# Kernel optimization log

Measured on AMD Instinct MI355X. Metric: run time of the kernel, lower is better.

Reference implementation:

```python
import jax, jax.numpy as jnp
import numpy as np

SCENE = (256, 256, 32)     # scene_size from SLCF-Net docstring (256*256*32 voxels)
PROJECT_SCALE = 1
C, H, W = 64, 480, 640
N = SCENE[0] * SCENE[1] * SCENE[2]


def setup_inputs() -> dict:
    key = jax.random.key(0)
    k1, k2, k3, k4, k5 = jax.random.split(key, 5)
    x2d = jax.random.normal(k1, (C, H, W), dtype=jnp.float32)
    # pix coords in [0, 480) -> valid for both x (<640) and y (<480)
    projected_pix = jax.random.randint(k2, (N, 2), 0, 480, dtype=jnp.int32)
    fov_mask = jax.random.bernoulli(k3, 0.7, (N,))
    pix_z = jax.random.uniform(k4, (N,), dtype=jnp.float32) * 50.0
    depth_img = jax.random.uniform(k5, (1, H, W), dtype=jnp.float32) * 50.0
    return {
        "x2d": x2d,
        "projected_pix": projected_pix,
        "scale_2d": 1,
        "fov_mask": fov_mask,
        "pix_z": pix_z,
        "depth_img": depth_img,
    }


def reference(x2d, projected_pix, scale_2d, fov_mask, pix_z, depth_img):
    c, h, w = x2d.shape
    pix_x = projected_pix[:, 0]
    pix_y = projected_pix[:, 1]

    # --- feature gather (out-of-FOV voxels map to the appended zero column) ---
    sx = pix_x // scale_2d
    sy = pix_y // scale_2d
    feat_idx = sy * w + sx                                  # (N,)
    src = x2d.reshape(c, -1)                                # (c, h*w)
    src_feature = jnp.where(fov_mask[None, :], src[:, feat_idx], jnp.float32(0.0))  # (c, N)

    # --- depth gather (out-of-FOV voxels map to the appended zero entry) ---
    dep_idx = pix_y * w + pix_x                             # (N,)
    depth_flat = depth_img.reshape(-1)                      # (h*w,)
    depth_values = jnp.where(fov_mask, depth_flat[dep_idx], jnp.float32(0.0))       # (N,)

    # --- gaussian decay weight, mu=0, sigma=1/project_scale; depth==0 -> weight 1 ---
    sigma = jnp.float32(1.0 / PROJECT_SCALE)
    gw = jnp.exp(jnp.float32(-0.5) * ((pix_z - depth_values) / sigma) ** 2)
    weights = jnp.where(depth_values == 0.0, jnp.float32(1.0), gw)                  # (N,)

    weighted = src_feature * weights[None, :]               # (c, N)
    s = PROJECT_SCALE
    return weighted.reshape(c, SCENE[0] // s, SCENE[1] // s, SCENE[2] // s)
```

## Files before the change

kernel.cpp:

```cpp
#include <hip/hip_runtime.h>
#include <hip/hip_bf16.h>

#define NVOX (256*256*32)
#define CC 64
#define HH 480
#define WW 640
#define HWTOT (HH*WW)

typedef float vfloat4 __attribute__((ext_vector_type(4)));
typedef int   vint4   __attribute__((ext_vector_type(4)));

__global__ __launch_bounds__(256) void weight_kernel(
    const int*   __restrict__ pp,
    const int*   __restrict__ scale_p,
    const int*   __restrict__ mask,
    const float* __restrict__ pix_z,
    const float* __restrict__ depth,
    int*         __restrict__ feat_out,
    float*       __restrict__ w_out)
{
    int t = blockIdx.x * blockDim.x + threadIdx.x;
    if (t * 4 >= NVOX) return;
    int scale = scale_p[0];

    vint4 pp0 = ((const vint4*)pp)[t*2+0];
    vint4 pp1 = ((const vint4*)pp)[t*2+1];
    vint4 m4  = ((const vint4*)mask)[t];
    vfloat4 z4 = ((const vfloat4*)pix_z)[t];

    int   px[4] = {pp0.x, pp0.z, pp1.x, pp1.z};
    int   py[4] = {pp0.y, pp0.w, pp1.y, pp1.w};
    int   mm[4] = {m4.x, m4.y, m4.z, m4.w};
    float zz[4] = {z4.x, z4.y, z4.z, z4.w};

    int fi[4]; float wv[4];
#pragma unroll
    for (int j = 0; j < 4; ++j) {
        int sx = px[j], sy = py[j];
        if (scale != 1) { sx = px[j] / scale; sy = py[j] / scale; }
        int feat = sy * WW + sx;
        bool fov = (mm[j] != 0);
        float d = fov ? depth[py[j] * WW + px[j]] : 0.0f;
        float diff = zz[j] - d;
        float gw = __expf(-0.5f * diff * diff);
        float w = (d == 0.0f) ? 1.0f : gw;
        wv[j] = fov ? w : 0.0f;
        fi[j] = fov ? feat : 0;
    }
    vint4 fo;  fo.x=fi[0]; fo.y=fi[1]; fo.z=fi[2]; fo.w=fi[3];
    vfloat4 wo; wo.x=wv[0]; wo.y=wv[1]; wo.z=wv[2]; wo.w=wv[3];
    ((vint4*)feat_out)[t] = fo;
    ((vfloat4*)w_out)[t]  = wo;
}

__global__ __launch_bounds__(256) void transpose_kernel(
    const float* __restrict__ x2d,
    float*       __restrict__ xT)
{
    __shared__ float tile[64][65];
    int t  = threadIdx.x;
    int p0 = blockIdx.x * 64;

#pragma unroll
    for (int k = 0; k < 16; ++k) {
        int c = k * 4 + (t >> 6);
        int p = t & 63;
        tile[c][p] = x2d[(long)c * HWTOT + p0 + p];
    }
    __syncthreads();
#pragma unroll
    for (int k = 0; k < 16; ++k) {
        int p = k * 4 + (t >> 6);
        int c = t & 63;
        xT[(long)(p0 + p) * CC + c] = tile[c][p];
    }
}

__global__ __launch_bounds__(256) void gather64_kernel(
    const float* __restrict__ xT,
    const int*   __restrict__ feat_idx,
    const float* __restrict__ wgt,
    float*       __restrict__ out)
{
    int i = blockIdx.x * blockDim.x + threadIdx.x;
    int fi  = __builtin_nontemporal_load(feat_idx + i);
    float w = __builtin_nontemporal_load(wgt + i);

    const vfloat4* src = (const vfloat4*)(xT + (long)fi * CC);
    float* op = out + i;

#pragma unroll
    for (int g = 0; g < 16; ++g) {
        vfloat4 v = src[g];
        v.x *= w; v.y *= w; v.z *= w; v.w *= w;
        __builtin_nontemporal_store(v.x, op + (long)(4*g + 0) * NVOX);
        __builtin_nontemporal_store(v.y, op + (long)(4*g + 1) * NVOX);
        __builtin_nontemporal_store(v.z, op + (long)(4*g + 2) * NVOX);
        __builtin_nontemporal_store(v.w, op + (long)(4*g + 3) * NVOX);
    }
}

__global__ __launch_bounds__(256) void scatter_kernel(
    const float* __restrict__ x2d,
    const int*   __restrict__ feat_idx,
    const float* __restrict__ wgt,
    float*       __restrict__ out)
{
    int t = blockIdx.x * blockDim.x + threadIdx.x;
    long i0 = (long)t * 4;
    int cg = blockIdx.y * 4;

    vint4   f4 = __builtin_nontemporal_load((const vint4*)feat_idx + t);
    vfloat4 w4 = __builtin_nontemporal_load((const vfloat4*)wgt + t);

#pragma unroll
    for (int g = 0; g < 4; ++g) {
        int c = cg + g;
        const float* base = x2d + (long)c * HWTOT;
        vfloat4 v;
        v.x = base[f4.x] * w4.x;
        v.y = base[f4.y] * w4.y;
        v.z = base[f4.z] * w4.z;
        v.w = base[f4.w] * w4.w;
        __builtin_nontemporal_store(v, (vfloat4*)(out + (long)c * NVOX + i0));
    }
}

__global__ __launch_bounds__(256) void fused_kernel(
    const float* __restrict__ x2d,
    const int*   __restrict__ pp,
    const int*   __restrict__ scale_p,
    const int*   __restrict__ mask,
    const float* __restrict__ pix_z,
    const float* __restrict__ depth,
    float*       __restrict__ out)
{
    int t = blockIdx.x * blockDim.x + threadIdx.x;
    long i0 = (long)t * 4;
    int cg = blockIdx.y * 4;
    int scale = scale_p[0];

    vint4 pp0 = ((const vint4*)pp)[t*2+0];
    vint4 pp1 = ((const vint4*)pp)[t*2+1];
    vint4 m4  = ((const vint4*)mask)[t];
    vfloat4 z4 = ((const vfloat4*)pix_z)[t];

    int   px[4] = {pp0.x, pp0.z, pp1.x, pp1.z};
    int   py[4] = {pp0.y, pp0.w, pp1.y, pp1.w};
    int   mm[4] = {m4.x, m4.y, m4.z, m4.w};
    float zz[4] = {z4.x, z4.y, z4.z, z4.w};

    int fi[4]; float wv[4];
#pragma unroll
    for (int j = 0; j < 4; ++j) {
        int sx = px[j], sy = py[j];
        if (scale != 1) { sx = px[j] / scale; sy = py[j] / scale; }
        int feat = sy * WW + sx;
        bool fov = (mm[j] != 0);
        float d = fov ? depth[py[j] * WW + px[j]] : 0.0f;
        float diff = zz[j] - d;
        float gw = __expf(-0.5f * diff * diff);
        float w = (d == 0.0f) ? 1.0f : gw;
        wv[j] = fov ? w : 0.0f;
        fi[j] = fov ? feat : 0;
    }

#pragma unroll
    for (int g = 0; g < 4; ++g) {
        int c = cg + g;
        const float* base = x2d + (long)c * HWTOT;
        vfloat4 v;
        v.x = base[fi[0]] * wv[0];
        v.y = base[fi[1]] * wv[1];
        v.z = base[fi[2]] * wv[2];
        v.w = base[fi[3]] * wv[3];
        __builtin_nontemporal_store(v, (vfloat4*)(out + (long)c * NVOX + i0));
    }
}

extern "C" void kernel_launch(void* const* d_in, const int* in_sizes, int n_in,
                              void* d_out, int out_size, void* d_ws, size_t ws_size,
                              hipStream_t stream) {
    const float* x2d     = (const float*)d_in[0];
    const int*   pp      = (const int*)d_in[1];
    const int*   scale_p = (const int*)d_in[2];
    const int*   mask    = (const int*)d_in[3];
    const float* pix_z   = (const float*)d_in[4];
    const float* depth   = (const float*)d_in[5];
    float*       out     = (float*)d_out;

    const int nquad = NVOX / 4;
    dim3 blk(256);

    size_t need_meta = (size_t)NVOX * 8;
    size_t need_full = need_meta + (size_t)HWTOT * CC * 4;

    if (ws_size >= need_full) {
        int*   feat_ws = (int*)d_ws;
        float* w_ws    = (float*)((char*)d_ws + (size_t)NVOX * 4);
        float* xT      = (float*)((char*)d_ws + need_meta);
        weight_kernel<<<dim3(nquad/256), blk, 0, stream>>>(pp, scale_p, mask,
                                                           pix_z, depth, feat_ws, w_ws);
        transpose_kernel<<<dim3(HWTOT/64), blk, 0, stream>>>(x2d, xT);
        gather64_kernel<<<dim3(NVOX/256), blk, 0, stream>>>(xT, feat_ws, w_ws, out);
    } else if (ws_size >= need_meta) {
        int*   feat_ws = (int*)d_ws;
        float* w_ws    = (float*)((char*)d_ws + (size_t)NVOX * 4);
        weight_kernel<<<dim3(nquad/256), blk, 0, stream>>>(pp, scale_p, mask,
                                                           pix_z, depth, feat_ws, w_ws);
        scatter_kernel<<<dim3(nquad/256, CC/4), blk, 0, stream>>>(x2d, feat_ws, w_ws, out);
    } else {
        fused_kernel<<<dim3(nquad/256, CC/4), blk, 0, stream>>>(x2d, pp, scale_p,
                                                                mask, pix_z, depth, out);
    }
}
```

Measured before the change: 663.0 us.

## Fuse weight computation into gather kernel and vectorize transpose loads/stores

Drops the separate weight/index kernel and computes each voxel's feature index and Gaussian depth weight inside the gather kernel. This avoids writing and re-reading two N-sized metadata arrays and saves one launch. The transpose kernel now uses float4 nontemporal loads and float4 stores, so each thread moves four values per access. Shared-memory reads in the transpose now stride across channels, which may cause some bank conflicts.

Result: slower. 688.6 us (+3.9%).

```diff
diff --git a/kernel.cpp b/kernel.cpp
--- a/kernel.cpp
+++ b/kernel.cpp
@@ -1,5 +1,4 @@
 #include <hip/hip_runtime.h>
-#include <hip/hip_bf16.h>
 
 #define NVOX (256*256*32)
 #define CC 64
@@ -9,49 +8,7 @@
 
 typedef float vfloat4 __attribute__((ext_vector_type(4)));
 typedef int   vint4   __attribute__((ext_vector_type(4)));
-
-__global__ __launch_bounds__(256) void weight_kernel(
-    const int*   __restrict__ pp,
-    const int*   __restrict__ scale_p,
-    const int*   __restrict__ mask,
-    const float* __restrict__ pix_z,
-    const float* __restrict__ depth,
-    int*         __restrict__ feat_out,
-    float*       __restrict__ w_out)
-{
-    int t = blockIdx.x * blockDim.x + threadIdx.x;
-    if (t * 4 >= NVOX) return;
-    int scale = scale_p[0];
-
-    vint4 pp0 = ((const vint4*)pp)[t*2+0];
-    vint4 pp1 = ((const vint4*)pp)[t*2+1];
-    vint4 m4  = ((const vint4*)mask)[t];
-    vfloat4 z4 = ((const vfloat4*)pix_z)[t];
-
-    int   px[4] = {pp0.x, pp0.z, pp1.x, pp1.z};
-    int   py[4] = {pp0.y, pp0.w, pp1.y, pp1.w};
-    int   mm[4] = {m4.x, m4.y, m4.z, m4.w};
-    float zz[4] = {z4.x, z4.y, z4.z, z4.w};
-
-    int fi[4]; float wv[4];
-#pragma unroll
-    for (int j = 0; j < 4; ++j) {
-        int sx = px[j], sy = py[j];
-        if (scale != 1) { sx = px[j] / scale; sy = py[j] / scale; }
-        int feat = sy * WW + sx;
-        bool fov = (mm[j] != 0);
-        float d = fov ? depth[py[j] * WW + px[j]] : 0.0f;
-        float diff = zz[j] - d;
-        float gw = __expf(-0.5f * diff * diff);
-        float w = (d == 0.0f) ? 1.0f : gw;
-        wv[j] = fov ? w : 0.0f;
-        fi[j] = fov ? feat : 0;
-    }
-    vint4 fo;  fo.x=fi[0]; fo.y=fi[1]; fo.z=fi[2]; fo.w=fi[3];
-    vfloat4 wo; wo.x=wv[0]; wo.y=wv[1]; wo.z=wv[2]; wo.w=wv[3];
-    ((vint4*)feat_out)[t] = fo;
-    ((vfloat4*)w_out)[t]  = wo;
-}
+typedef int   vint2   __attribute__((ext_vector_type(2)));
 
 __global__ __launch_bounds__(256) void transpose_kernel(
     const float* __restrict__ x2d,
@@ -62,29 +19,58 @@
     int p0 = blockIdx.x * 64;
 
 #pragma unroll
-    for (int k = 0; k < 16; ++k) {
-        int c = k * 4 + (t >> 6);
-        int p = t & 63;
-        tile[c][p] = x2d[(long)c * HWTOT + p0 + p];
+    for (int k = 0; k < 4; ++k) {
+        int idx = k * 256 + t;
+        int c   = idx >> 4;
+        int pg  = idx & 15;
+        vfloat4 v = __builtin_nontemporal_load(
+            (const vfloat4*)(x2d + (long)c * HWTOT + p0) + pg);
+        tile[c][pg*4+0] = v.x;
+        tile[c][pg*4+1] = v.y;
+        tile[c][pg*4+2] = v.z;
+        tile[c][pg*4+3] = v.w;
     }
     __syncthreads();
 #pragma unroll
-    for (int k = 0; k < 16; ++k) {
-        int p = k * 4 + (t >> 6);
-        int c = t & 63;
-        xT[(long)(p0 + p) * CC + c] = tile[c][p];
+    for (int k = 0; k < 4; ++k) {
+        int idx = k * 256 + t;
+        int p   = idx >> 4;
+        int cg  = idx & 15;
+        vfloat4 v;
+        v.x = tile[cg*4+0][p];
+        v.y = tile[cg*4+1][p];
+        v.z = tile[cg*4+2][p];
+        v.w = tile[cg*4+3][p];
+        ((vfloat4*)(xT + (long)(p0 + p) * CC))[cg] = v;
     }
 }
 
-__global__ __launch_bounds__(256) void gather64_kernel(
+__global__ __launch_bounds__(256) void gather_fused_kernel(
     const float* __restrict__ xT,
-    const int*   __restrict__ feat_idx,
-    const float* __restrict__ wgt,
+    const int*   __restrict__ pp,
+    const int*   __restrict__ scale_p,
+    const int*   __restrict__ mask,
+    const float* __restrict__ pix_z,
+    const float* __restrict__ depth,
     float*       __restrict__ out)
 {
     int i = blockIdx.x * blockDim.x + threadIdx.x;
-    int fi  = __builtin_nontemporal_load(feat_idx + i);
-    float w = __builtin_nontemporal_load(wgt + i);
+    int scale = scale_p[0];
+
+    vint2 p2 = __builtin_nontemporal_load((const vint2*)pp + i);
+    int   m  = __builtin_nontemporal_load(mask + i);
+    float z  = __builtin_nontemporal_load(pix_z + i);
+
+    int px = p2.x, py = p2.y;
+    int sx = px, sy = py;
+    if (scale != 1) { sx = px / scale; sy = py / scale; }
+    bool fov = (m != 0);
+    int  fi  = fov ? (sy * WW + sx) : 0;
+    float d  = fov ? depth[py * WW + px] : 0.0f;
+    float diff = z - d;
+    float gw = __expf(-0.5f * diff * diff);
+    float w  = (d == 0.0f) ? 1.0f : gw;
+    w = fov ? w : 0.0f;
 
     const vfloat4* src = (const vfloat4*)(xT + (long)fi * CC);
     float* op = out + i;
@@ -97,32 +83,6 @@
         __builtin_nontemporal_store(v.y, op + (long)(4*g + 1) * NVOX);
         __builtin_nontemporal_store(v.z, op + (long)(4*g + 2) * NVOX);
         __builtin_nontemporal_store(v.w, op + (long)(4*g + 3) * NVOX);
-    }
-}
-
-__global__ __launch_bounds__(256) void scatter_kernel(
-    const float* __restrict__ x2d,
-    const int*   __restrict__ feat_idx,
-    const float* __restrict__ wgt,
-    float*       __restrict__ out)
-{
-    int t = blockIdx.x * blockDim.x + threadIdx.x;
-    long i0 = (long)t * 4;
-    int cg = blockIdx.y * 4;
-
-    vint4   f4 = __builtin_nontemporal_load((const vint4*)feat_idx + t);
-    vfloat4 w4 = __builtin_nontemporal_load((const vfloat4*)wgt + t);
-
-#pragma unroll
-    for (int g = 0; g < 4; ++g) {
-        int c = cg + g;
-        const float* base = x2d + (long)c * HWTOT;
-        vfloat4 v;
-        v.x = base[f4.x] * w4.x;
-        v.y = base[f4.y] * w4.y;
-        v.z = base[f4.z] * w4.z;
-        v.w = base[f4.w] * w4.w;
-        __builtin_nontemporal_store(v, (vfloat4*)(out + (long)c * NVOX + i0));
     }
 }
 
@@ -189,28 +149,16 @@
     const float* depth   = (const float*)d_in[5];
     float*       out     = (float*)d_out;
 
-    const int nquad = NVOX / 4;
     dim3 blk(256);
+    size_t need_xT = (size_t)HWTOT * CC * 4;
 
-    size_t need_meta = (size_t)NVOX * 8;
-    size_t need_full = need_meta + (size_t)HWTOT * CC * 4;
-
-    if (ws_size >= need_full) {
-        int*   feat_ws = (int*)d_ws;
-        float* w_ws    = (float*)((char*)d_ws + (size_t)NVOX * 4);
-        float* xT      = (float*)((char*)d_ws + need_meta);
-        weight_kernel<<<dim3(nquad/256), blk, 0, stream>>>(pp, scale_p, mask,
-                                                           pix_z, depth, feat_ws, w_ws);
+    if (ws_size >= need_xT) {
+        float* xT = (float*)d_ws;
         transpose_kernel<<<dim3(HWTOT/64), blk, 0, stream>>>(x2d, xT);
-        gather64_kernel<<<dim3(NVOX/256), blk, 0, stream>>>(xT, feat_ws, w_ws, out);
-    } else if (ws_size >= need_meta) {
-        int*   feat_ws = (int*)d_ws;
-        float* w_ws    = (float*)((char*)d_ws + (size_t)NVOX * 4);
-        weight_kernel<<<dim3(nquad/256), blk, 0, stream>>>(pp, scale_p, mask,
-                                                           pix_z, depth, feat_ws, w_ws);
-        scatter_kernel<<<dim3(nquad/256, CC/4), blk, 0, stream>>>(x2d, feat_ws, w_ws, out);
+        gather_fused_kernel<<<dim3(NVOX/256), blk, 0, stream>>>(xT, pp, scale_p,
+                                                                mask, pix_z, depth, out);
     } else {
-        fused_kernel<<<dim3(nquad/256, CC/4), blk, 0, stream>>>(x2d, pp, scale_p,
-                                                                mask, pix_z, depth, out);
+        fused_kernel<<<dim3(NVOX/4/256, CC/4), blk, 0, stream>>>(x2d, pp, scale_p,
+                                                                 mask, pix_z, depth, out);
     }
 }
```
